# Kernel tuning notes

Measured on AMD Instinct MI355X. Metric: run time of the kernel, lower is better.

The kernel has to match this reference:

```python
import jax, jax.numpy as jnp
import numpy as np

N_LEVELS = 16
N_FEATS = 2
LOG2_HASH = 19
HASH_SIZE = 1 << LOG2_HASH
BASE_RES = 16
FINEST_RES = 512
_b = np.exp((np.log(FINEST_RES) - np.log(BASE_RES)) / (N_LEVELS - 1))
RESOLUTIONS = [int(np.ceil(BASE_RES * _b ** i)) for i in range(N_LEVELS)]
PRIMES = jnp.array([1, 2654435761, 805459861], dtype=jnp.uint32)
# all 8 corner offsets of a voxel, ordered (i,j,k) like the torch triple loop
OFFSETS = jnp.array([[i, j, k] for i in range(2) for j in range(2) for k in range(2)], dtype=jnp.int32)  # (8,3)


def _hash(corners):
    # corners: (..., 3) int32. Matches torch int64 (c0*p0 ^ c1*p1 ^ c2*p2) % 2^19:
    # XOR and mod-2^19 depend only on low bits, so uint32 arithmetic is exact.
    c = corners.astype(jnp.uint32) * PRIMES  # (...,3)
    h = c[..., 0] ^ c[..., 1] ^ c[..., 2]
    return (h & jnp.uint32(HASH_SIZE - 1)).astype(jnp.int32)


def setup_inputs() -> dict:
    key = jax.random.key(0)
    kx, kt = jax.random.split(key)
    x = jax.random.uniform(kx, (2097152, 3), dtype=jnp.float32)
    tables = jax.random.normal(kt, (N_LEVELS, HASH_SIZE, N_FEATS), dtype=jnp.float32) * 0.01
    return {"x": x, "tables": tables}


def reference(x, tables):
    x = jnp.clip(x, 0.0, 1.0 - 1e-6)  # (N,3)
    outs = []
    for level, res in enumerate(RESOLUTIONS):
        scaled = x * res                                # (N,3)
        floor = jnp.floor(scaled)
        w = scaled - floor                              # (N,3) trilinear frac
        floor_i = floor.astype(jnp.int32)
        corners = floor_i[:, None, :] + OFFSETS[None, :, :]   # (N,8,3)
        idx = _hash(corners)                            # (N,8)
        feats = tables[level][idx]                      # (N,8,F) hash gather
        # per-corner trilinear weight: prod over dims of (w if offset else 1-w)
        cw = jnp.where(OFFSETS[None, :, :] == 1, w[:, None, :], 1.0 - w[:, None, :])  # (N,8,3)
        cw = cw[:, :, 0] * cw[:, :, 1] * cw[:, :, 2]    # (N,8)
        outs.append(jnp.einsum('nc,ncf->nf', cw, feats))  # (N,F)
    return jnp.concatenate(outs, axis=-1)               # (N, L*F)
```

## Files before the change

kernel.cpp:

```cpp
#include <hip/hip_runtime.h>
#include <math.h>

#define NL 16
#define NFINE 8
#define HASH_SIZE (1u << 19)
#define HASH_MASK (HASH_SIZE - 1u)
#define P1 2654435761u
#define P2 805459861u
#define PTS_PER_BLOCK 1024
#define THREADS 256
#define BX 32
#define NB (BX * BX * BX)
#define SCAN_BLOCKS (NB / THREADS)

typedef float f2 __attribute__((ext_vector_type(2)));
typedef float f4 __attribute__((ext_vector_type(4)));

struct Res16 { float r[NL]; };

__device__ __forceinline__ void clamp3(float& px, float& py, float& pz)
{
    px = fminf(fmaxf(px, 0.0f), 0.999999f);
    py = fminf(fmaxf(py, 0.0f), 0.999999f);
    pz = fminf(fmaxf(pz, 0.0f), 0.999999f);
}

__device__ __forceinline__ f2 enc_pl_simple(const f2* __restrict__ tb, float r,
                                            float px, float py, float pz)
{
    float sx = px * r, sy = py * r, sz = pz * r;
    float fx = floorf(sx), fy = floorf(sy), fz = floorf(sz);
    float wx = sx - fx, wy = sy - fy, wz = sz - fz;
    unsigned ix = (unsigned)(int)fx;
    unsigned iy = (unsigned)(int)fy;
    unsigned iz = (unsigned)(int)fz;
    unsigned hx0 = ix,      hx1 = ix + 1u;
    unsigned hy0 = iy * P1, hy1 = hy0 + P1;
    unsigned hz0 = iz * P2, hz1 = hz0 + P2;

    f2 f000 = tb[(hx0 ^ hy0 ^ hz0) & HASH_MASK];
    f2 f001 = tb[(hx0 ^ hy0 ^ hz1) & HASH_MASK];
    f2 f010 = tb[(hx0 ^ hy1 ^ hz0) & HASH_MASK];
    f2 f011 = tb[(hx0 ^ hy1 ^ hz1) & HASH_MASK];
    f2 f100 = tb[(hx1 ^ hy0 ^ hz0) & HASH_MASK];
    f2 f101 = tb[(hx1 ^ hy0 ^ hz1) & HASH_MASK];
    f2 f110 = tb[(hx1 ^ hy1 ^ hz0) & HASH_MASK];
    f2 f111 = tb[(hx1 ^ hy1 ^ hz1) & HASH_MASK];

    float wx0 = 1.0f - wx, wy0 = 1.0f - wy, wz0 = 1.0f - wz;
    float c000 = (wx0 * wy0) * wz0, c001 = (wx0 * wy0) * wz;
    float c010 = (wx0 * wy ) * wz0, c011 = (wx0 * wy ) * wz;
    float c100 = (wx  * wy0) * wz0, c101 = (wx  * wy0) * wz;
    float c110 = (wx  * wy ) * wz0, c111 = (wx  * wy ) * wz;

    float a0 = c000 * f000.x + c001 * f001.x + c010 * f010.x + c011 * f011.x
             + c100 * f100.x + c101 * f101.x + c110 * f110.x + c111 * f111.x;
    float a1 = c000 * f000.y + c001 * f001.y + c010 * f010.y + c011 * f011.y
             + c100 * f100.y + c101 * f101.y + c110 * f110.y + c111 * f111.y;
    f2 ret; ret.x = a0; ret.y = a1;
    return ret;
}

__device__ __forceinline__ f2 enc_pl_merged(const f2* __restrict__ tb, float r,
                                            float px, float py, float pz)
{
    float sx = px * r, sy = py * r, sz = pz * r;
    float fx = floorf(sx), fy = floorf(sy), fz = floorf(sz);
    float wx = sx - fx, wy = sy - fy, wz = sz - fz;
    unsigned ix = (unsigned)(int)fx;
    unsigned iy = (unsigned)(int)fy;
    unsigned iz = (unsigned)(int)fz;
    unsigned hy0 = iy * P1, hy1 = hy0 + P1;
    unsigned hz0 = iz * P2, hz1 = hz0 + P2;
    f2 f000, f001, f010, f011, f100, f101, f110, f111;
    if ((ix & 1u) == 0u) {
        const f4* __restrict__ tb4 = reinterpret_cast<const f4*>(tb);
        unsigned g00 = (ix ^ hy0 ^ hz0) & HASH_MASK;
        unsigned g01 = (ix ^ hy0 ^ hz1) & HASH_MASK;
        unsigned g10 = (ix ^ hy1 ^ hz0) & HASH_MASK;
        unsigned g11 = (ix ^ hy1 ^ hz1) & HASH_MASK;
        f4 v00 = tb4[g00 >> 1]; f4 v01 = tb4[g01 >> 1];
        f4 v10 = tb4[g10 >> 1]; f4 v11 = tb4[g11 >> 1];
        f2 lo, hi;
        lo.x = v00.x; lo.y = v00.y; hi.x = v00.z; hi.y = v00.w;
        f000 = (g00 & 1u) ? hi : lo;  f100 = (g00 & 1u) ? lo : hi;
        lo.x = v01.x; lo.y = v01.y; hi.x = v01.z; hi.y = v01.w;
        f001 = (g01 & 1u) ? hi : lo;  f101 = (g01 & 1u) ? lo : hi;
        lo.x = v10.x; lo.y = v10.y; hi.x = v10.z; hi.y = v10.w;
        f010 = (g10 & 1u) ? hi : lo;  f110 = (g10 & 1u) ? lo : hi;
        lo.x = v11.x; lo.y = v11.y; hi.x = v11.z; hi.y = v11.w;
        f011 = (g11 & 1u) ? hi : lo;  f111 = (g11 & 1u) ? lo : hi;
    } else {
        unsigned hx0 = ix, hx1 = ix + 1u;
        f000 = tb[(hx0 ^ hy0 ^ hz0) & HASH_MASK];
        f001 = tb[(hx0 ^ hy0 ^ hz1) & HASH_MASK];
        f010 = tb[(hx0 ^ hy1 ^ hz0) & HASH_MASK];
        f011 = tb[(hx0 ^ hy1 ^ hz1) & HASH_MASK];
        f100 = tb[(hx1 ^ hy0 ^ hz0) & HASH_MASK];
        f101 = tb[(hx1 ^ hy0 ^ hz1) & HASH_MASK];
        f110 = tb[(hx1 ^ hy1 ^ hz0) & HASH_MASK];
        f111 = tb[(hx1 ^ hy1 ^ hz1) & HASH_MASK];
    }
    float wx0 = 1.0f - wx, wy0 = 1.0f - wy, wz0 = 1.0f - wz;
    float c000 = (wx0 * wy0) * wz0, c001 = (wx0 * wy0) * wz;
    float c010 = (wx0 * wy ) * wz0, c011 = (wx0 * wy ) * wz;
    float c100 = (wx  * wy0) * wz0, c101 = (wx  * wy0) * wz;
    float c110 = (wx  * wy ) * wz0, c111 = (wx  * wy ) * wz;
    float a0 = c000 * f000.x + c001 * f001.x + c010 * f010.x + c011 * f011.x
             + c100 * f100.x + c101 * f101.x + c110 * f110.x + c111 * f111.x;
    float a1 = c000 * f000.y + c001 * f001.y + c010 * f010.y + c011 * f011.y
             + c100 * f100.y + c101 * f101.y + c110 * f110.y + c111 * f111.y;
    f2 ret; ret.x = a0; ret.y = a1;
    return ret;
}

__global__ __launch_bounds__(THREADS) void hist_kernel(
    const float* __restrict__ x, int* __restrict__ hist, int N)
{
    __shared__ int lh[NB];
    for (int i = threadIdx.x; i < NB; i += THREADS) lh[i] = 0;
    __syncthreads();
    for (int n = blockIdx.x * THREADS + threadIdx.x; n < N;
         n += gridDim.x * THREADS) {
        float px = x[3 * (size_t)n + 0];
        float py = x[3 * (size_t)n + 1];
        float pz = x[3 * (size_t)n + 2];
        clamp3(px, py, pz);
        int bin = ((int)(pz * BX) * BX + (int)(py * BX)) * BX + (int)(px * BX);
        atomicAdd(&lh[bin], 1);
    }
    __syncthreads();
    for (int i = threadIdx.x; i < NB; i += THREADS)
        if (lh[i]) atomicAdd(&hist[i], lh[i]);
}

__global__ __launch_bounds__(THREADS) void scan1_kernel(
    const int* __restrict__ hist, int* __restrict__ bsum)
{
    __shared__ int sm[THREADS];
    int t = threadIdx.x;
    sm[t] = hist[blockIdx.x * THREADS + t];
    __syncthreads();
    for (int off = THREADS / 2; off > 0; off >>= 1) {
        if (t < off) sm[t] += sm[t + off];
        __syncthreads();
    }
    if (t == 0) bsum[blockIdx.x] = sm[0];
}

__global__ __launch_bounds__(SCAN_BLOCKS) void scan2_kernel(
    const int* __restrict__ bsum, int* __restrict__ bpre)
{
    __shared__ int sm[SCAN_BLOCKS];
    int t = threadIdx.x;
    int v = bsum[t];
    sm[t] = v;
    __syncthreads();
    for (int off = 1; off < SCAN_BLOCKS; off <<= 1) {
        int u = (t >= off) ? sm[t - off] : 0;
        __syncthreads();
        sm[t] += u;
        __syncthreads();
    }
    bpre[t] = sm[t] - v;
}

__global__ __launch_bounds__(THREADS) void scan3_kernel(
    const int* __restrict__ hist, const int* __restrict__ bpre,
    int* __restrict__ cursor)
{
    __shared__ int sm[THREADS];
    int t = threadIdx.x;
    int v = hist[blockIdx.x * THREADS + t];
    sm[t] = v;
    __syncthreads();
    for (int off = 1; off < THREADS; off <<= 1) {
        int u = (t >= off) ? sm[t - off] : 0;
        __syncthreads();
        sm[t] += u;
        __syncthreads();
    }
    cursor[blockIdx.x * THREADS + t] = bpre[blockIdx.x] + sm[t] - v;
}

__global__ __launch_bounds__(THREADS) void scatter_kernel(
    const float* __restrict__ x, int* __restrict__ cursor,
    float* __restrict__ sx, int* __restrict__ perm, int N)
{
    int n = blockIdx.x * THREADS + threadIdx.x;
    if (n >= N) return;
    float px = x[3 * (size_t)n + 0];
    float py = x[3 * (size_t)n + 1];
    float pz = x[3 * (size_t)n + 2];
    clamp3(px, py, pz);
    int bin = ((int)(pz * BX) * BX + (int)(py * BX)) * BX + (int)(px * BX);
    int pos = atomicAdd(&cursor[bin], 1);
    f4 v; v.x = px; v.y = py; v.z = pz; v.w = 0.0f;
    *reinterpret_cast<f4*>(sx + (size_t)pos * 4) = v;
    perm[pos] = n;
}

__global__ __launch_bounds__(THREADS) void hashenc_fine_all_kernel(
    const float* __restrict__ sx, const float* __restrict__ tables,
    float* __restrict__ ws, int N, int nchunks, Res16 res)
{
    int level = 8 + blockIdx.x / nchunks;
    int chunk = blockIdx.x % nchunks;
    float r = res.r[level];
    const f2* __restrict__ tb =
        reinterpret_cast<const f2*>(tables) + (size_t)level * HASH_SIZE;
    f2* __restrict__ wl =
        reinterpret_cast<f2*>(ws) + (size_t)(level - 8) * N;
    int base = chunk * PTS_PER_BLOCK + threadIdx.x;
#pragma unroll
    for (int i = 0; i < PTS_PER_BLOCK / THREADS; ++i) {
        int n = base + i * THREADS;
        if (n >= N) break;
        f4 p = *reinterpret_cast<const f4*>(sx + (size_t)n * 4);
        f2 a = enc_pl_merged(tb, r, p.x, p.y, p.z);
        wl[n] = a;
    }
}

__global__ __launch_bounds__(THREADS) void hashenc_transpose_fused_kernel(
    const float* __restrict__ ws,
    const float* __restrict__ sx,
    const int* __restrict__ perm,
    const float* __restrict__ tables,
    float* __restrict__ out, int N, Res16 res)
{
    int c    = threadIdx.x & 7;
    int pid  = threadIdx.x >> 3;
    int lane = threadIdx.x & 63;
    int base = blockIdx.x * 256;
    const f2* __restrict__ w2 = reinterpret_cast<const f2*>(ws);
    const f2* __restrict__ tbc =
        reinterpret_cast<const f2*>(tables) + (size_t)c * HASH_SIZE;
    float rc = res.r[c];
    int srcA = (lane & ~7) | ((2 * c) & 7);
    int srcB = srcA + 1;
#pragma unroll
    for (int i = 0; i < 8; ++i) {
        int p  = base + i * 32 + pid;
        int pc = p < N ? p : N - 1;
        f4 pt = *reinterpret_cast<const f4*>(sx + (size_t)pc * 4);
        f2 mine = enc_pl_simple(tbc, rc, pt.x, pt.y, pt.z);
        float Ax = __shfl(mine.x, srcA, 64);
        float Ay = __shfl(mine.y, srcA, 64);
        float Bx = __shfl(mine.x, srcB, 64);
        float By = __shfl(mine.y, srcB, 64);
        f4 v;
        if (c < 4) {
            v.x = Ax; v.y = Ay; v.z = Bx; v.w = By;
        } else {
            f2 a = w2[(size_t)(2 * c - 8) * N + pc];
            f2 b = w2[(size_t)(2 * c - 7) * N + pc];
            v.x = a.x; v.y = a.y; v.z = b.x; v.w = b.y;
        }
        if (p < N) {
            int o = perm[p];
            __builtin_nontemporal_store(
                v, reinterpret_cast<f4*>(out + (size_t)o * (2 * NL) + c * 4));
        }
    }
}

__global__ __launch_bounds__(THREADS) void hashenc_level_nosort_kernel(
    const float* __restrict__ x, const float* __restrict__ tables,
    float* __restrict__ ws, int N, int nchunks, Res16 res)
{
    int slot  = blockIdx.x & 7;
    int rest  = blockIdx.x >> 3;
    int chunk = rest % nchunks;
    int phase = rest / nchunks;
    int level = phase * 8 + slot;
    float r = res.r[level];
    const f2* __restrict__ tb =
        reinterpret_cast<const f2*>(tables) + (size_t)level * HASH_SIZE;
    f2* __restrict__ wl = reinterpret_cast<f2*>(ws) + (size_t)level * N;
    int base = chunk * PTS_PER_BLOCK + threadIdx.x;
#pragma unroll
    for (int i = 0; i < PTS_PER_BLOCK / THREADS; ++i) {
        int n = base + i * THREADS;
        if (n >= N) break;
        float px = __builtin_nontemporal_load(x + 3 * (size_t)n + 0);
        float py = __builtin_nontemporal_load(x + 3 * (size_t)n + 1);
        float pz = __builtin_nontemporal_load(x + 3 * (size_t)n + 2);
        clamp3(px, py, pz);
        f2 a = enc_pl_merged(tb, r, px, py, pz);
        __builtin_nontemporal_store(a, wl + n);
    }
}

__global__ __launch_bounds__(THREADS) void hashenc_transpose_nosort_kernel(
    const float* __restrict__ ws, float* __restrict__ out, int N)
{
    int c    = threadIdx.x & 7;
    int pid  = threadIdx.x >> 3;
    int base = blockIdx.x * 256;
    const f2* __restrict__ w2 = reinterpret_cast<const f2*>(ws);
#pragma unroll
    for (int i = 0; i < 8; ++i) {
        int p = base + i * 32 + pid;
        if (p >= N) return;
        f2 a = __builtin_nontemporal_load(w2 + (size_t)(2 * c)     * N + p);
        f2 b = __builtin_nontemporal_load(w2 + (size_t)(2 * c + 1) * N + p);
        f4 v; v.x = a.x; v.y = a.y; v.z = b.x; v.w = b.y;
        __builtin_nontemporal_store(
            v, reinterpret_cast<f4*>(out + (size_t)p * (2 * NL) + c * 4));
    }
}

__global__ __launch_bounds__(THREADS) void hashenc_mono_kernel(
    const float* __restrict__ x, const float* __restrict__ tables,
    float* __restrict__ out, int N, Res16 res)
{
    int n = blockIdx.x * THREADS + threadIdx.x;
    if (n >= N) return;
    float px = x[3 * (size_t)n + 0], py = x[3 * (size_t)n + 1], pz = x[3 * (size_t)n + 2];
    clamp3(px, py, pz);
    float acc[2 * NL];
#pragma unroll
    for (int l = 0; l < NL; ++l) {
        const f2* tb = reinterpret_cast<const f2*>(tables) + (size_t)l * HASH_SIZE;
        f2 a = enc_pl_merged(tb, res.r[l], px, py, pz);
        acc[2 * l] = a.x; acc[2 * l + 1] = a.y;
    }
    f4* o = reinterpret_cast<f4*>(out + (size_t)n * (2 * NL));
#pragma unroll
    for (int q = 0; q < 8; ++q) {
        f4 v; v.x = acc[4*q]; v.y = acc[4*q+1]; v.z = acc[4*q+2]; v.w = acc[4*q+3];
        o[q] = v;
    }
}

extern "C" void kernel_launch(void* const* d_in, const int* in_sizes, int n_in,
                              void* d_out, int out_size, void* d_ws, size_t ws_size,
                              hipStream_t stream)
{
    const float* x      = (const float*)d_in[0];
    const float* tables = (const float*)d_in[1];
    float* out          = (float*)d_out;
    int N = in_sizes[0] / 3;

    Res16 res;
    double b = exp((log(512.0) - log(16.0)) / 15.0);
    for (int i = 0; i < NL; ++i)
        res.r[i] = (float)(int)ceil(16.0 * pow(b, (double)i));

    size_t enc_f      = (size_t)NFINE * N * 2;
    size_t need_sort  = (enc_f + (size_t)N * 5 + 2 * NB + 2 * SCAN_BLOCKS) * sizeof(float);
    size_t need_plain = (size_t)NL * N * 2 * sizeof(float);

    if (ws_size >= need_sort) {
        float* wse    = (float*)d_ws;
        float* sx     = wse + enc_f;
        int*   perm   = (int*)(sx + (size_t)N * 4);
        int*   hist   = perm + N;
        int*   cursor = hist + NB;
        int*   bsum   = cursor + NB;
        int*   bpre   = bsum + SCAN_BLOCKS;

        hipMemsetAsync(hist, 0, NB * sizeof(int), stream);
        hipLaunchKernelGGL(hist_kernel, dim3(256), dim3(THREADS), 0, stream,
                           x, hist, N);
        hipLaunchKernelGGL(scan1_kernel, dim3(SCAN_BLOCKS), dim3(THREADS), 0, stream,
                           hist, bsum);
        hipLaunchKernelGGL(scan2_kernel, dim3(1), dim3(SCAN_BLOCKS), 0, stream,
                           bsum, bpre);
        hipLaunchKernelGGL(scan3_kernel, dim3(SCAN_BLOCKS), dim3(THREADS), 0, stream,
                           hist, bpre, cursor);
        hipLaunchKernelGGL(scatter_kernel, dim3((N + THREADS - 1) / THREADS),
                           dim3(THREADS), 0, stream, x, cursor, sx, perm, N);

        int nchunks = (N + PTS_PER_BLOCK - 1) / PTS_PER_BLOCK;
        hipLaunchKernelGGL(hashenc_fine_all_kernel, dim3(8 * nchunks),
                           dim3(THREADS), 0, stream, sx, tables, wse, N,
                           nchunks, res);
        hipLaunchKernelGGL(hashenc_transpose_fused_kernel, dim3((N + 255) / 256),
                           dim3(THREADS), 0, stream, wse, sx, perm, tables, out,
                           N, res);
    } else if (ws_size >= need_plain) {
        int nchunks = (N + PTS_PER_BLOCK - 1) / PTS_PER_BLOCK;
        hipLaunchKernelGGL(hashenc_level_nosort_kernel, dim3(2 * 8 * nchunks),
                           dim3(THREADS), 0, stream, x, tables, (float*)d_ws,
                           N, nchunks, res);
        hipLaunchKernelGGL(hashenc_transpose_nosort_kernel, dim3((N + 255) / 256),
                           dim3(THREADS), 0, stream, (const float*)d_ws, out, N);
    } else {
        hipLaunchKernelGGL(hashenc_mono_kernel, dim3((N + THREADS - 1) / THREADS),
                           dim3(THREADS), 0, stream, x, tables, out, N, res);
    }
}
```

Baseline: 687.4 us.

## Reorder fine-level points within block by sub-bin parity to improve gather locality

In the fine-level kernel, each block now stages its 1024 points in shared memory and buckets them into 8 classes by the parity of their 64-resolution cell coordinates. The bucketing uses shared-memory atomics and a small prefix sum, and the point index is carried in the w component. Threads then process the points in bucket order and scatter results back to their original index. The aim is to group points so that consecutive threads touch more similar hash-table entries, improving cache behavior. The cost is extra synchronisation, shared-memory traffic and scattered output writes.

```diff
diff --git a/kernel.cpp b/kernel.cpp
--- a/kernel.cpp
+++ b/kernel.cpp
@@ -204,6 +204,9 @@
     const float* __restrict__ sx, const float* __restrict__ tables,
     float* __restrict__ ws, int N, int nchunks, Res16 res)
 {
+    __shared__ f4 pts[PTS_PER_BLOCK];
+    __shared__ int bh[8];
+    __shared__ int bb[8];
     int level = 8 + blockIdx.x / nchunks;
     int chunk = blockIdx.x % nchunks;
     float r = res.r[level];
@@ -211,14 +214,56 @@
         reinterpret_cast<const f2*>(tables) + (size_t)level * HASH_SIZE;
     f2* __restrict__ wl =
         reinterpret_cast<f2*>(ws) + (size_t)(level - 8) * N;
-    int base = chunk * PTS_PER_BLOCK + threadIdx.x;
-#pragma unroll
-    for (int i = 0; i < PTS_PER_BLOCK / THREADS; ++i) {
-        int n = base + i * THREADS;
-        if (n >= N) break;
-        f4 p = *reinterpret_cast<const f4*>(sx + (size_t)n * 4);
-        f2 a = enc_pl_merged(tb, r, p.x, p.y, p.z);
-        wl[n] = a;
+    int cbase = chunk * PTS_PER_BLOCK;
+    int count = N - cbase;
+    if (count > PTS_PER_BLOCK) count = PTS_PER_BLOCK;
+
+    if (threadIdx.x < 8) bh[threadIdx.x] = 0;
+    __syncthreads();
+
+    f4 p[4];
+    int k[4];
+#pragma unroll
+    for (int i = 0; i < 4; ++i) {
+        int idx = threadIdx.x + i * THREADS;
+        k[i] = -1;
+        if (idx < count) {
+            f4 q = *reinterpret_cast<const f4*>(sx + (size_t)(cbase + idx) * 4);
+            int kx = ((int)(q.x * 64.0f)) & 1;
+            int ky = ((int)(q.y * 64.0f)) & 1;
+            int kz = ((int)(q.z * 64.0f)) & 1;
+            int key = (kz << 2) | (ky << 1) | kx;
+            q.w = __int_as_float(cbase + idx);
+            p[i] = q;
+            k[i] = key;
+            atomicAdd(&bh[key], 1);
+        }
+    }
+    __syncthreads();
+    if (threadIdx.x == 0) {
+        int run = 0;
+#pragma unroll
+        for (int q8 = 0; q8 < 8; ++q8) { bb[q8] = run; run += bh[q8]; }
+    }
+    __syncthreads();
+    if (threadIdx.x < 8) bh[threadIdx.x] = bb[threadIdx.x];
+    __syncthreads();
+#pragma unroll
+    for (int i = 0; i < 4; ++i) {
+        if (k[i] >= 0) {
+            int pos = atomicAdd(&bh[k[i]], 1);
+            pts[pos] = p[i];
+        }
+    }
+    __syncthreads();
+#pragma unroll
+    for (int i = 0; i < 4; ++i) {
+        int j = threadIdx.x + i * THREADS;
+        if (j < count) {
+            f4 q = pts[j];
+            f2 a = enc_pl_merged(tb, r, q.x, q.y, q.z);
+            wl[__float_as_int(q.w)] = a;
+        }
     }
 }
 
```

After: 728.3 us. +6.0%, slower.
